# Optimization experiments

Measured on AMD Instinct MI355X. Metric: run time of the kernel, lower is better.

Reference implementation:

```python
import jax, jax.numpy as jnp
import numpy as np

HEADS = 8
EMBED = 64  # out_channels per head
N_OP = 100000
N_MC = 20000
N_EDGE = 300000
EPS = 1e-16  # matches PyG softmax denominator epsilon


def hetero_gat(x_src, x_dst, edge_index, W, att, n_dst):
    """GAT conv: gather -> per-edge score -> segment softmax over dst -> scatter-sum -> head mean.
    x_src: [Ns, F], x_dst: [Nd, F], edge_index: [2, E] (row0=src, row1=dst),
    W: [HEADS*EMBED, F], att: [1, HEADS, 2*EMBED].
    """
    hs = (x_src @ W.T).reshape(-1, HEADS, EMBED)  # [Ns,H,C]
    hd = (x_dst @ W.T).reshape(-1, HEADS, EMBED)  # [Nd,H,C]
    src, dst = edge_index[0], edge_index[1]
    x_j = hs[src]                                  # [E,H,C] (source/neighbor)
    x_i = hd[dst]                                  # [E,H,C] (destination)
    att_i = att[0, :, :EMBED]                      # [H,C] weights for x_i part of concat
    att_j = att[0, :, EMBED:]                      # [H,C] weights for x_j part
    # (cat([x_i,x_j],-1) * att).sum(-1) without materializing the concat
    alpha = jnp.einsum('ehc,hc->eh', x_i, att_i) + jnp.einsum('ehc,hc->eh', x_j, att_j)
    # segment softmax grouped by destination node
    m = jax.ops.segment_max(alpha, dst, num_segments=n_dst)  # [Nd,H]
    e = jnp.exp(alpha - m[dst])
    s = jax.ops.segment_sum(e, dst, num_segments=n_dst)      # [Nd,H]
    alpha = e / (s[dst] + EPS)                                # [E,H]
    msg = x_j * alpha[..., None]                              # [E,H,C]
    out = jax.ops.segment_sum(msg, dst, num_segments=n_dst)   # [Nd,H,C]
    return out.mean(axis=1)                                   # [Nd,C] multi-head mean


def setup_inputs() -> dict:
    key = jax.random.key(0)
    ks = jax.random.split(key, 12)
    op_nodes = jax.random.normal(ks[0], (N_OP, 4), dtype=jnp.float32)
    mc_nodes = jax.random.normal(ks[1], (N_MC, 2), dtype=jnp.float32)
    src = jax.random.randint(ks[2], (N_EDGE,), 0, N_OP)
    dst = jax.random.randint(ks[3], (N_EDGE,), 0, N_MC)
    edge_index_om = jnp.stack([src, dst]).astype(jnp.int64)
    g = 0.1
    params = {
        'W_op': jax.random.normal(ks[4], (EMBED, 4), dtype=jnp.float32) * g,
        'b_op': jnp.zeros((EMBED,), dtype=jnp.float32),
        'W_mc': jax.random.normal(ks[5], (EMBED, 2), dtype=jnp.float32) * g,
        'b_mc': jnp.zeros((EMBED,), dtype=jnp.float32),
        'W_om': jax.random.normal(ks[6], (HEADS * EMBED, EMBED), dtype=jnp.float32) * g,
        'att_om': jax.random.normal(ks[7], (1, HEADS, 2 * EMBED), dtype=jnp.float32) * g,
        'W_mo': jax.random.normal(ks[8], (HEADS * EMBED, EMBED), dtype=jnp.float32) * g,
        'att_mo': jax.random.normal(ks[9], (1, HEADS, 2 * EMBED), dtype=jnp.float32) * g,
    }
    return {'op_nodes': op_nodes, 'mc_nodes': mc_nodes, 'edge_index_om': edge_index_om, **params}


def reference(op_nodes, mc_nodes, edge_index_om, W_op, b_op, W_mc, b_mc,
              W_om, att_om, W_mo, att_mo):
    h_op = jax.nn.elu(op_nodes @ W_op.T + b_op)   # [N_OP, 64]
    h_mc = jax.nn.elu(mc_nodes @ W_mc.T + b_mc)   # [N_MC, 64]
    # op -> mc
    h_mc_new = hetero_gat(h_op, h_mc, edge_index_om, W_om, att_om, N_MC)
    h_mc = jax.nn.elu(h_mc + h_mc_new)
    # mc -> op (reversed edges)
    edge_index_mo = jnp.stack([edge_index_om[1], edge_index_om[0]])
    h_op_new = hetero_gat(h_mc, h_op, edge_index_mo, W_mo, att_mo, N_OP)
    h_op = jax.nn.elu(h_op + h_op_new)
    return (h_op, h_mc)
```

## Files before the change

kernel.cpp:

```cpp
#include <hip/hip_runtime.h>
#include <hip/hip_bf16.h>

using bf16 = __hip_bfloat16;
typedef __attribute__((ext_vector_type(8))) short short8;
typedef __attribute__((ext_vector_type(4))) float f32x4;

__device__ __forceinline__ unsigned short f2bf(float f) {
  bf16 h = __float2bfloat16(f);
  return *reinterpret_cast<unsigned short*>(&h);
}
__device__ __forceinline__ float bf2f(unsigned short u) {
  return __uint_as_float(((unsigned)u) << 16);
}

__device__ __forceinline__ float loadf(const void* p, int i, int is_f32) {
  if (is_f32) return ((const float*)p)[i];
  return __bfloat162float(((const bf16*)p)[i]);
}

__global__ __launch_bounds__(256) void init_kernel(
    const int* __restrict__ ei, const unsigned short* __restrict__ x,
    int* __restrict__ flags, int* __restrict__ cnt1, int n1,
    int* __restrict__ cnt2, int n2) {
  int t = threadIdx.x;
  int g = blockIdx.x * 256 + t;
  int stride = gridDim.x * 256;
  for (int i = g; i < n1; i += stride) cnt1[i] = 0;
  for (int i = g; i < n2; i += stride) cnt2[i] = 0;
  if (blockIdx.x == 0) {
    __shared__ int red[256];
    int o = 0, big = 0;
    for (int i = t; i < 2048; i += 256) {
      o |= ei[2 * i + 1];
      float v = __uint_as_float(((unsigned)x[2 * i]) << 16);
      if (!(fabsf(v) < 1000.f)) big = 1;
    }
    red[t] = o;
    __syncthreads();
    for (int d = 128; d > 0; d >>= 1) {
      if (t < d) red[t] |= red[t + d];
      __syncthreads();
    }
    int o_all = red[0];
    __syncthreads();
    red[t] = big;
    __syncthreads();
    for (int d = 128; d > 0; d >>= 1) {
      if (t < d) red[t] |= red[t + d];
      __syncthreads();
    }
    if (t == 0) {
      flags[0] = red[0];
      flags[1] = (o_all == 0) ? 1 : 0;
    }
  }
}

__device__ __forceinline__ int edge_src(const int* ei, int E, int e, int i64) {
  return i64 ? ei[2 * e] : ei[e];
}
__device__ __forceinline__ int edge_dst(const int* ei, int E, int e, int i64) {
  return i64 ? ei[2 * E + 2 * e] : ei[E + e];
}

template <int FIN>
__device__ __forceinline__ void node_body(
    const void* x, const void* W, const void* b, int is_f32,
    const float* vj, bf16* h_out, float* ea_out, int n) {
  int lane = threadIdx.x & 63;
  float acc = loadf(b, lane, is_f32);
#pragma unroll
  for (int f = 0; f < FIN; ++f)
    acc += loadf(x, n * FIN + f, is_f32) * loadf(W, lane * FIN + f, is_f32);
  float hv = acc > 0.f ? acc : expm1f(acc);
  h_out[(size_t)n * 64 + lane] = __float2bfloat16(hv);
  if (ea_out) {
    float p[8];
#pragma unroll
    for (int h = 0; h < 8; ++h) p[h] = hv * vj[h * 64 + lane];
#pragma unroll
    for (int i = 0; i < 4; ++i) {
      float send = (lane & 4) ? p[i] : p[i + 4];
      float keep = (lane & 4) ? p[i + 4] : p[i];
      p[i] = keep + __shfl_xor(send, 4, 64);
    }
#pragma unroll
    for (int i = 0; i < 2; ++i) {
      float send = (lane & 2) ? p[i] : p[i + 2];
      float keep = (lane & 2) ? p[i + 2] : p[i];
      p[i] = keep + __shfl_xor(send, 2, 64);
    }
    {
      float send = (lane & 1) ? p[0] : p[1];
      float keep = (lane & 1) ? p[1] : p[0];
      p[0] = keep + __shfl_xor(send, 1, 64);
    }
    p[0] += __shfl_xor(p[0], 8, 64);
    p[0] += __shfl_xor(p[0], 16, 64);
    p[0] += __shfl_xor(p[0], 32, 64);
    if (lane < 8) ea_out[(size_t)n * 8 + lane] = __expf(p[0]);
  }
}

__global__ __launch_bounds__(256) void front_kernel(
    const void* __restrict__ x_op, const void* __restrict__ W_op,
    const void* __restrict__ b_op, const void* __restrict__ x_mc,
    const void* __restrict__ W_mc, const void* __restrict__ b_mc,
    const void* __restrict__ W1, const void* __restrict__ att1,
    const void* __restrict__ W2, const void* __restrict__ att2,
    const int* __restrict__ ei, const int* __restrict__ flags,
    float* __restrict__ vj1, bf16* __restrict__ Wrt1, float* __restrict__ vj2,
    bf16* __restrict__ Wrt2, bf16* __restrict__ h_op,
    float* __restrict__ ea_op, bf16* __restrict__ h_mc,
    int* __restrict__ cnt_dst, int* __restrict__ cnt_src, int n_op, int n_mc,
    int E, int nbo, int nbm) {
  int bid = blockIdx.x;
  int is_f32 = flags[0];
  if (bid < nbo) {
    int n = bid * 4 + (threadIdx.x >> 6);
    if (n < n_op) node_body<4>(x_op, W_op, b_op, is_f32, vj1, h_op, ea_op, n);
  } else if (bid < nbo + nbm) {
    int n = (bid - nbo) * 4 + (threadIdx.x >> 6);
    if (n < n_mc)
      node_body<2>(x_mc, W_mc, b_mc, is_f32, nullptr, h_mc, nullptr, n);
  } else if (bid < nbo + nbm + 256) {
    int pb = bid - nbo - nbm;
    int side = pb >= 128;
    const void* W = side ? W2 : W1;
    const void* att = side ? att2 : att1;
    float* vj = side ? vj2 : vj1;
    bf16* Wrt = side ? Wrt2 : Wrt1;
    int tt = (pb & 127) * 256 + threadIdx.x;
    if (tt < 32768) {
      int c = tt >> 9, k = tt & 511;
      int f = k >> 3, h = k & 7;
      Wrt[tt] = __float2bfloat16(loadf(W, ((h << 6) + c) * 64 + f, is_f32));
    }
    if (tt < 512) {
      int hh = tt >> 6, ff = tt & 63;
      float s = 0.f;
      for (int cc = 0; cc < 64; ++cc)
        s += loadf(att, hh * 128 + 64 + cc, is_f32) *
             loadf(W, ((hh << 6) + cc) * 64 + ff, is_f32);
      vj[tt] = s;
    }
  } else {
    int i64 = flags[1];
    int e = (bid - nbo - nbm - 256) * 256 + threadIdx.x;
    if (e < E) {
      atomicAdd(&cnt_dst[edge_dst(ei, E, e, i64)], 1);
      atomicAdd(&cnt_src[edge_src(ei, E, e, i64)], 1);
    }
  }
}

__global__ __launch_bounds__(256) void scan_bsum2(
    const int* __restrict__ cnt1, int n1, int nb1, const int* __restrict__ cnt2,
    int n2, int* __restrict__ bsum1, int* __restrict__ bsum2) {
  __shared__ int red[256];
  int t = threadIdx.x;
  int side = (int)blockIdx.x >= nb1;
  const int* cnt = side ? cnt2 : cnt1;
  int n = side ? n2 : n1;
  int blk = side ? (blockIdx.x - nb1) : blockIdx.x;
  int base = blk * 2048 + t * 8;
  int s = 0;
#pragma unroll
  for (int i = 0; i < 8; ++i)
    if (base + i < n) s += cnt[base + i];
  red[t] = s;
  __syncthreads();
  for (int d = 128; d > 0; d >>= 1) {
    if (t < d) red[t] += red[t + d];
    __syncthreads();
  }
  if (t == 0) (side ? bsum2 : bsum1)[blk] = red[0];
}

__global__ __launch_bounds__(256) void scan_write2(
    const int* __restrict__ cnt1, int n1, int nb1,
    const int* __restrict__ bsum1, int* __restrict__ offs1,
    int* __restrict__ cur1, const int* __restrict__ cnt2, int n2, int nb2,
    const int* __restrict__ bsum2, int* __restrict__ offs2,
    int* __restrict__ cur2) {
  __shared__ int red[256];
  __shared__ int base_s;
  int t = threadIdx.x;
  int side = (int)blockIdx.x >= nb1;
  const int* cnt = side ? cnt2 : cnt1;
  const int* bsum = side ? bsum2 : bsum1;
  int* offs = side ? offs2 : offs1;
  int* cur = side ? cur2 : cur1;
  int n = side ? n2 : n1;
  int nb = side ? nb2 : nb1;
  int blk = side ? (blockIdx.x - nb1) : blockIdx.x;
  if (t == 0) {
    int b = 0;
    for (int i = 0; i < blk; ++i) b += bsum[i];
    base_s = b;
  }
  int base = blk * 2048 + t * 8;
  int c[8];
  int s = 0;
#pragma unroll
  for (int i = 0; i < 8; ++i) {
    c[i] = (base + i < n) ? cnt[base + i] : 0;
    s += c[i];
  }
  red[t] = s;
  __syncthreads();
  for (int d = 1; d < 256; d <<= 1) {
    int v = red[t];
    int add = (t >= d) ? red[t - d] : 0;
    __syncthreads();
    red[t] = v + add;
    __syncthreads();
  }
  int run = base_s + red[t] - s;
#pragma unroll
  for (int i = 0; i < 8; ++i) {
    if (base + i < n) {
      offs[base + i] = run;
      cur[base + i] = run;
      run += c[i];
    }
  }
  if (blk == nb - 1 && t == 255) offs[n] = base_s + red[255];
}

__global__ __launch_bounds__(256) void fill_edges(
    const int* __restrict__ ei, int E, const int* __restrict__ flags,
    int* __restrict__ cur1, int* __restrict__ srcs1, int* __restrict__ cur2,
    int* __restrict__ srcs2) {
  int i64 = flags[1];
  int e = blockIdx.x * blockDim.x + threadIdx.x;
  if (e < E) {
    int s = edge_src(ei, E, e, i64), d = edge_dst(ei, E, e, i64);
    int p = atomicAdd(&cur1[d], 1);
    srcs1[p] = s;
    int q = atomicAdd(&cur2[s], 1);
    srcs2[q] = d;
  }
}

template <bool WRITE_AJ, bool WRITE_BF>
__global__ __launch_bounds__(256) void gat_fused(
    int Nd, const int* __restrict__ offs, const int* __restrict__ srcs,
    const float* __restrict__ ea, const bf16* __restrict__ h_src,
    const bf16* __restrict__ Wrt, const bf16* __restrict__ h_res,
    float* __restrict__ out_f32, bf16* __restrict__ out_bf,
    const float* __restrict__ vj_next, float* __restrict__ ea_next) {
  __shared__ __align__(16) unsigned short Zl[16 * 520];
  __shared__ int srcs_sw[4][65];
  __shared__ __align__(16) float ew_s[4][520];
  __shared__ float ajp[4][16][8];

  int t = threadIdx.x;
  int wv = t >> 6, lane = t & 63;
  int d0 = blockIdx.x * 16;
  int sj = lane >> 4;
  int fq = lane & 15;

  int dlo = d0 + wv * 4;
  int wo0 = offs[min(dlo + 0, Nd)];
  int wo1 = offs[min(dlo + 1, Nd)];
  int wo2 = offs[min(dlo + 2, Nd)];
  int wo3 = offs[min(dlo + 3, Nd)];
  int wo4 = offs[min(dlo + 4, Nd)];
  int woj = sj == 0 ? wo0 : sj == 1 ? wo1 : sj == 2 ? wo2 : wo3;
  int woj1 = sj == 0 ? wo1 : sj == 1 ? wo2 : sj == 2 ? wo3 : wo4;

  float z[8][4];
#pragma unroll
  for (int h = 0; h < 8; ++h)
#pragma unroll
    for (int f = 0; f < 4; ++f) z[h][f] = 0.f;
  float s8[8];
#pragma unroll
  for (int h = 0; h < 8; ++h) s8[h] = 0.f;

  for (int cb = wo0; cb < wo4; cb += 64) {
    int cn = min(64, wo4 - cb);
    for (int i = lane; i < cn + 1; i += 64)
      srcs_sw[wv][i] = (i < cn) ? srcs[cb + i] : 0;
    for (int i = lane; i < (cn + 1) * 8; i += 64) {
      int e = i >> 3;
      ew_s[wv][i] =
          (e < cn) ? ea[(size_t)srcs_sw[wv][e] * 8 + (i & 7)] : 0.f;
    }
    int c0 = max(cb, woj) - cb;
    int e1 = min(cb + cn, woj1) - cb;
    int rl = max(e1 - c0, 0);
    int rmax = max(rl, __shfl_xor(rl, 16, 64));
    rmax = max(rmax, __shfl_xor(rmax, 32, 64));
    for (int r = 0; r < rmax; ++r) {
      int i2 = (r < rl) ? (c0 + r) : cn;
      int src = srcs_sw[wv][i2];
      ushort4 u = *(const ushort4*)((const unsigned short*)h_src +
                                    (size_t)src * 64 + fq * 4);
      float x0 = bf2f(u.x), x1 = bf2f(u.y), x2 = bf2f(u.z), x3 = bf2f(u.w);
      float4 lo4 = *(const float4*)&ew_s[wv][i2 * 8];
      float4 hi4 = *(const float4*)&ew_s[wv][i2 * 8 + 4];
      z[0][0] += lo4.x * x0; z[0][1] += lo4.x * x1; z[0][2] += lo4.x * x2; z[0][3] += lo4.x * x3;
      z[1][0] += lo4.y * x0; z[1][1] += lo4.y * x1; z[1][2] += lo4.y * x2; z[1][3] += lo4.y * x3;
      z[2][0] += lo4.z * x0; z[2][1] += lo4.z * x1; z[2][2] += lo4.z * x2; z[2][3] += lo4.z * x3;
      z[3][0] += lo4.w * x0; z[3][1] += lo4.w * x1; z[3][2] += lo4.w * x2; z[3][3] += lo4.w * x3;
      z[4][0] += hi4.x * x0; z[4][1] += hi4.x * x1; z[4][2] += hi4.x * x2; z[4][3] += hi4.x * x3;
      z[5][0] += hi4.y * x0; z[5][1] += hi4.y * x1; z[5][2] += hi4.y * x2; z[5][3] += hi4.y * x3;
      z[6][0] += hi4.z * x0; z[6][1] += hi4.z * x1; z[6][2] += hi4.z * x2; z[6][3] += hi4.z * x3;
      z[7][0] += hi4.w * x0; z[7][1] += hi4.w * x1; z[7][2] += hi4.w * x2; z[7][3] += hi4.w * x3;
      s8[0] += lo4.x; s8[1] += lo4.y; s8[2] += lo4.z; s8[3] += lo4.w;
      s8[4] += hi4.x; s8[5] += hi4.y; s8[6] += hi4.z; s8[7] += hi4.w;
    }
  }

  float si[8];
#pragma unroll
  for (int h = 0; h < 8; ++h) si[h] = s8[h] > 0.f ? 1.f / s8[h] : 0.f;
  int row = wv * 4 + sj;
#pragma unroll
  for (int fi = 0; fi < 4; ++fi) {
    int4 pk;
    pk.x = ((int)f2bf(z[1][fi] * si[1]) << 16) | f2bf(z[0][fi] * si[0]);
    pk.y = ((int)f2bf(z[3][fi] * si[3]) << 16) | f2bf(z[2][fi] * si[2]);
    pk.z = ((int)f2bf(z[5][fi] * si[5]) << 16) | f2bf(z[4][fi] * si[4]);
    pk.w = ((int)f2bf(z[7][fi] * si[7]) << 16) | f2bf(z[6][fi] * si[6]);
    *(int4*)&Zl[row * 520 + (fq * 4 + fi) * 8] = pk;
  }
  __syncthreads();

  int arow = lane & 15;
  int kg = lane >> 4;
  f32x4 acc = {0.f, 0.f, 0.f, 0.f};
#pragma unroll
  for (int kt = 0; kt < 16; ++kt) {
    int kbase = kt * 32 + kg * 8;
    short8 a = *(const short8*)&Zl[arow * 520 + kbase];
    short8 b = *(const short8*)&Wrt[(size_t)(wv * 16 + arow) * 512 + kbase];
    acc = __builtin_amdgcn_mfma_f32_16x16x32_bf16(a, b, acc, 0, 0, 0);
  }

  int col = wv * 16 + arow;
  float o_r[4];
#pragma unroll
  for (int r = 0; r < 4; ++r) {
    int dloc = kg * 4 + r;
    int d = d0 + dloc;
    float o = 0.f;
    if (d < Nd) {
      float v = __bfloat162float(h_res[(size_t)d * 64 + col]) + 0.125f * acc[r];
      o = v > 0.f ? v : expm1f(v);
      out_f32[(size_t)d * 64 + col] = o;
      if (WRITE_BF) out_bf[(size_t)d * 64 + col] = __float2bfloat16(o);
    }
    o_r[r] = o;
  }

  if (WRITE_AJ) {
#pragma unroll
    for (int r = 0; r < 4; ++r) {
      int dloc = kg * 4 + r;
      float p[8];
#pragma unroll
      for (int h = 0; h < 8; ++h) p[h] = o_r[r] * vj_next[h * 64 + col];
#pragma unroll
      for (int i = 0; i < 4; ++i) {
        float send = (arow & 4) ? p[i] : p[i + 4];
        float keep = (arow & 4) ? p[i + 4] : p[i];
        p[i] = keep + __shfl_xor(send, 4, 64);
      }
#pragma unroll
      for (int i = 0; i < 2; ++i) {
        float send = (arow & 2) ? p[i] : p[i + 2];
        float keep = (arow & 2) ? p[i + 2] : p[i];
        p[i] = keep + __shfl_xor(send, 2, 64);
      }
      {
        float send = (arow & 1) ? p[0] : p[1];
        float keep = (arow & 1) ? p[1] : p[0];
        p[0] = keep + __shfl_xor(send, 1, 64);
      }
      p[0] += __shfl_xor(p[0], 8, 64);
      if (arow < 8) ajp[wv][dloc][arow] = p[0];
    }
    __syncthreads();
    if (t < 128) {
      int dloc = t >> 3, h = t & 7;
      int d = d0 + dloc;
      if (d < Nd) {
        float s = ajp[0][dloc][h] + ajp[1][dloc][h] + ajp[2][dloc][h] +
                  ajp[3][dloc][h];
        ea_next[(size_t)d * 8 + h] = __expf(s);
      }
    }
  }
}

extern "C" void kernel_launch(void* const* d_in, const int* in_sizes, int n_in,
                              void* d_out, int out_size, void* d_ws,
                              size_t ws_size, hipStream_t stream) {
  const void* op_nodes = d_in[0];
  const void* mc_nodes = d_in[1];
  const int* ei        = (const int*)d_in[2];
  const void* W_op     = d_in[3];
  const void* b_op     = d_in[4];
  const void* W_mc     = d_in[5];
  const void* b_mc     = d_in[6];
  const void* W_om     = d_in[7];
  const void* att_om   = d_in[8];
  const void* W_mo     = d_in[9];
  const void* att_mo   = d_in[10];

  int n_op = in_sizes[0] / 4;
  int n_mc = in_sizes[1] / 2;
  int E    = in_sizes[2] / 2;

  char* ws = (char*)d_ws;
  size_t off = 0;
  auto alloc = [&](size_t bytes) -> void* {
    void* p = ws + off;
    off = (off + bytes + 255) & ~(size_t)255;
    return p;
  };
  int* flags   = (int*)alloc(16);
  bf16* h_op   = (bf16*)alloc((size_t)n_op * 64 * 2);
  bf16* h_mc   = (bf16*)alloc((size_t)n_mc * 64 * 2);
  bf16* h_mc2  = (bf16*)alloc((size_t)n_mc * 64 * 2);
  float* ea_op = (float*)alloc((size_t)n_op * 8 * 4);
  float* ea_mc = (float*)alloc((size_t)n_mc * 8 * 4);
  float* vj_om = (float*)alloc(512 * 4);
  float* vj_mo = (float*)alloc(512 * 4);
  bf16* Wrt_om = (bf16*)alloc(32768 * 2);
  bf16* Wrt_mo = (bf16*)alloc(32768 * 2);
  int* cnt1  = (int*)alloc((size_t)n_mc * 4);
  int* cnt2  = (int*)alloc((size_t)n_op * 4);
  int* offs1 = (int*)alloc((size_t)(n_mc + 1) * 4);
  int* cur1  = (int*)alloc((size_t)n_mc * 4);
  int* srcs1 = (int*)alloc((size_t)E * 4);
  int* offs2 = (int*)alloc((size_t)(n_op + 1) * 4);
  int* cur2  = (int*)alloc((size_t)n_op * 4);
  int* srcs2 = (int*)alloc((size_t)E * 4);
  int* bsum1 = (int*)alloc(256 * 4);
  int* bsum2 = (int*)alloc(256 * 4);

  float* out_op = (float*)d_out;
  float* out_mc = out_op + (size_t)n_op * 64;

  init_kernel<<<512, 256, 0, stream>>>(ei, (const unsigned short*)op_nodes,
                                       flags, cnt1, n_mc, cnt2, n_op);

  int nbo = (n_op + 3) / 4, nbm = (n_mc + 3) / 4;
  int nbe = (E + 255) / 256;
  front_kernel<<<nbo + nbm + 256 + nbe, 256, 0, stream>>>(
      op_nodes, W_op, b_op, mc_nodes, W_mc, b_mc, W_om, att_om, W_mo, att_mo,
      ei, flags, vj_om, Wrt_om, vj_mo, Wrt_mo, h_op, ea_op, h_mc, cnt1, cnt2,
      n_op, n_mc, E, nbo, nbm);

  int nb1 = (n_mc + 2047) / 2048, nb2 = (n_op + 2047) / 2048;
  scan_bsum2<<<nb1 + nb2, 256, 0, stream>>>(cnt1, n_mc, nb1, cnt2, n_op, bsum1,
                                            bsum2);
  scan_write2<<<nb1 + nb2, 256, 0, stream>>>(cnt1, n_mc, nb1, bsum1, offs1,
                                             cur1, cnt2, n_op, nb2, bsum2,
                                             offs2, cur2);
  fill_edges<<<nbe, 256, 0, stream>>>(ei, E, flags, cur1, srcs1, cur2, srcs2);

  gat_fused<true, true><<<(n_mc + 15) / 16, 256, 0, stream>>>(
      n_mc, offs1, srcs1, ea_op, h_op, Wrt_om, h_mc, out_mc, h_mc2, vj_mo,
      ea_mc);
  gat_fused<false, false><<<(n_op + 15) / 16, 256, 0, stream>>>(
      n_op, offs2, srcs2, ea_mc, h_mc2, Wrt_mo, h_op, out_op, (bf16*)nullptr,
      (const float*)nullptr, (float*)nullptr);
}
```

Before: 240.2 us.

## Batch node work per wave, batch gathers in GAT loop, reuse shared memory

Result: faster. 233.5 us (-2.8%).

```diff
diff --git a/kernel.cpp b/kernel.cpp
--- a/kernel.cpp
+++ b/kernel.cpp
@@ -64,41 +64,55 @@
 }
 
 template <int FIN>
-__device__ __forceinline__ void node_body(
+__device__ __forceinline__ void node_body4(
     const void* x, const void* W, const void* b, int is_f32,
-    const float* vj, bf16* h_out, float* ea_out, int n) {
+    const float* vj, bf16* h_out, float* ea_out, int n0, int N) {
   int lane = threadIdx.x & 63;
-  float acc = loadf(b, lane, is_f32);
-#pragma unroll
-  for (int f = 0; f < FIN; ++f)
-    acc += loadf(x, n * FIN + f, is_f32) * loadf(W, lane * FIN + f, is_f32);
-  float hv = acc > 0.f ? acc : expm1f(acc);
-  h_out[(size_t)n * 64 + lane] = __float2bfloat16(hv);
+  float wreg[FIN];
+#pragma unroll
+  for (int f = 0; f < FIN; ++f) wreg[f] = loadf(W, lane * FIN + f, is_f32);
+  float bias = loadf(b, lane, is_f32);
+  float vjreg[8];
   if (ea_out) {
-    float p[8];
-#pragma unroll
-    for (int h = 0; h < 8; ++h) p[h] = hv * vj[h * 64 + lane];
-#pragma unroll
-    for (int i = 0; i < 4; ++i) {
-      float send = (lane & 4) ? p[i] : p[i + 4];
-      float keep = (lane & 4) ? p[i + 4] : p[i];
-      p[i] = keep + __shfl_xor(send, 4, 64);
-    }
-#pragma unroll
-    for (int i = 0; i < 2; ++i) {
-      float send = (lane & 2) ? p[i] : p[i + 2];
-      float keep = (lane & 2) ? p[i + 2] : p[i];
-      p[i] = keep + __shfl_xor(send, 2, 64);
-    }
-    {
-      float send = (lane & 1) ? p[0] : p[1];
-      float keep = (lane & 1) ? p[1] : p[0];
-      p[0] = keep + __shfl_xor(send, 1, 64);
-    }
-    p[0] += __shfl_xor(p[0], 8, 64);
-    p[0] += __shfl_xor(p[0], 16, 64);
-    p[0] += __shfl_xor(p[0], 32, 64);
-    if (lane < 8) ea_out[(size_t)n * 8 + lane] = __expf(p[0]);
+#pragma unroll
+    for (int h = 0; h < 8; ++h) vjreg[h] = vj[h * 64 + lane];
+  }
+#pragma unroll
+  for (int j = 0; j < 4; ++j) {
+    int n = n0 + j;
+    if (n >= N) break;
+    float acc = bias;
+#pragma unroll
+    for (int f = 0; f < FIN; ++f)
+      acc += loadf(x, n * FIN + f, is_f32) * wreg[f];
+    float hv = acc > 0.f ? acc : expm1f(acc);
+    h_out[(unsigned)(n << 6) + lane] = __float2bfloat16(hv);
+    if (ea_out) {
+      float p[8];
+#pragma unroll
+      for (int h = 0; h < 8; ++h) p[h] = hv * vjreg[h];
+#pragma unroll
+      for (int i = 0; i < 4; ++i) {
+        float send = (lane & 4) ? p[i] : p[i + 4];
+        float keep = (lane & 4) ? p[i + 4] : p[i];
+        p[i] = keep + __shfl_xor(send, 4, 64);
+      }
+#pragma unroll
+      for (int i = 0; i < 2; ++i) {
+        float send = (lane & 2) ? p[i] : p[i + 2];
+        float keep = (lane & 2) ? p[i + 2] : p[i];
+        p[i] = keep + __shfl_xor(send, 2, 64);
+      }
+      {
+        float send = (lane & 1) ? p[0] : p[1];
+        float keep = (lane & 1) ? p[1] : p[0];
+        p[0] = keep + __shfl_xor(send, 1, 64);
+      }
+      p[0] += __shfl_xor(p[0], 8, 64);
+      p[0] += __shfl_xor(p[0], 16, 64);
+      p[0] += __shfl_xor(p[0], 32, 64);
+      if (lane < 8) ea_out[(unsigned)(n << 3) + lane] = __expf(p[0]);
+    }
   }
 }
 
@@ -117,12 +131,13 @@
   int bid = blockIdx.x;
   int is_f32 = flags[0];
   if (bid < nbo) {
-    int n = bid * 4 + (threadIdx.x >> 6);
-    if (n < n_op) node_body<4>(x_op, W_op, b_op, is_f32, vj1, h_op, ea_op, n);
+    int n0 = bid * 16 + (threadIdx.x >> 6) * 4;
+    if (n0 < n_op)
+      node_body4<4>(x_op, W_op, b_op, is_f32, vj1, h_op, ea_op, n0, n_op);
   } else if (bid < nbo + nbm) {
-    int n = (bid - nbo) * 4 + (threadIdx.x >> 6);
-    if (n < n_mc)
-      node_body<2>(x_mc, W_mc, b_mc, is_f32, nullptr, h_mc, nullptr, n);
+    int n0 = (bid - nbo) * 16 + (threadIdx.x >> 6) * 4;
+    if (n0 < n_mc)
+      node_body4<2>(x_mc, W_mc, b_mc, is_f32, nullptr, h_mc, nullptr, n0, n_mc);
   } else if (bid < nbo + nbm + 256) {
     int pb = bid - nbo - nbm;
     int side = pb >= 128;
@@ -252,8 +267,8 @@
     const float* __restrict__ vj_next, float* __restrict__ ea_next) {
   __shared__ __align__(16) unsigned short Zl[16 * 520];
   __shared__ int srcs_sw[4][65];
-  __shared__ __align__(16) float ew_s[4][520];
-  __shared__ float ajp[4][16][8];
+  __shared__ __align__(16) float ew_s[4][528];
+  float(*ajp)[16][8] = reinterpret_cast<float(*)[16][8]>(&ew_s[0][0]);
 
   int t = threadIdx.x;
   int wv = t >> 6, lane = t & 63;
@@ -279,38 +294,51 @@
 #pragma unroll
   for (int h = 0; h < 8; ++h) s8[h] = 0.f;
 
+  const unsigned short* hsrc_u = (const unsigned short*)h_src;
+
   for (int cb = wo0; cb < wo4; cb += 64) {
     int cn = min(64, wo4 - cb);
     for (int i = lane; i < cn + 1; i += 64)
       srcs_sw[wv][i] = (i < cn) ? srcs[cb + i] : 0;
     for (int i = lane; i < (cn + 1) * 8; i += 64) {
       int e = i >> 3;
-      ew_s[wv][i] =
-          (e < cn) ? ea[(size_t)srcs_sw[wv][e] * 8 + (i & 7)] : 0.f;
+      int src2 = (e < cn) ? srcs[cb + e] : 0;
+      ew_s[wv][i] = (e < cn) ? ea[((unsigned)src2 << 3) + (i & 7)] : 0.f;
     }
     int c0 = max(cb, woj) - cb;
     int e1 = min(cb + cn, woj1) - cb;
     int rl = max(e1 - c0, 0);
     int rmax = max(rl, __shfl_xor(rl, 16, 64));
     rmax = max(rmax, __shfl_xor(rmax, 32, 64));
-    for (int r = 0; r < rmax; ++r) {
-      int i2 = (r < rl) ? (c0 + r) : cn;
-      int src = srcs_sw[wv][i2];
-      ushort4 u = *(const ushort4*)((const unsigned short*)h_src +
-                                    (size_t)src * 64 + fq * 4);
-      float x0 = bf2f(u.x), x1 = bf2f(u.y), x2 = bf2f(u.z), x3 = bf2f(u.w);
-      float4 lo4 = *(const float4*)&ew_s[wv][i2 * 8];
-      float4 hi4 = *(const float4*)&ew_s[wv][i2 * 8 + 4];
-      z[0][0] += lo4.x * x0; z[0][1] += lo4.x * x1; z[0][2] += lo4.x * x2; z[0][3] += lo4.x * x3;
-      z[1][0] += lo4.y * x0; z[1][1] += lo4.y * x1; z[1][2] += lo4.y * x2; z[1][3] += lo4.y * x3;
-      z[2][0] += lo4.z * x0; z[2][1] += lo4.z * x1; z[2][2] += lo4.z * x2; z[2][3] += lo4.z * x3;
-      z[3][0] += lo4.w * x0; z[3][1] += lo4.w * x1; z[3][2] += lo4.w * x2; z[3][3] += lo4.w * x3;
-      z[4][0] += hi4.x * x0; z[4][1] += hi4.x * x1; z[4][2] += hi4.x * x2; z[4][3] += hi4.x * x3;
-      z[5][0] += hi4.y * x0; z[5][1] += hi4.y * x1; z[5][2] += hi4.y * x2; z[5][3] += hi4.y * x3;
-      z[6][0] += hi4.z * x0; z[6][1] += hi4.z * x1; z[6][2] += hi4.z * x2; z[6][3] += hi4.z * x3;
-      z[7][0] += hi4.w * x0; z[7][1] += hi4.w * x1; z[7][2] += hi4.w * x2; z[7][3] += hi4.w * x3;
-      s8[0] += lo4.x; s8[1] += lo4.y; s8[2] += lo4.z; s8[3] += lo4.w;
-      s8[4] += hi4.x; s8[5] += hi4.y; s8[6] += hi4.z; s8[7] += hi4.w;
+    for (int r0 = 0; r0 < rmax; r0 += 4) {
+      int i2q[4];
+      ushort4 uq[4];
+#pragma unroll
+      for (int q = 0; q < 4; ++q) {
+        int r = r0 + q;
+        int i2 = (r < rl) ? (c0 + r) : cn;
+        i2q[q] = i2;
+        int src = srcs_sw[wv][i2];
+        uq[q] = *(const ushort4*)(hsrc_u + (((unsigned)src) << 6) + (fq << 2));
+      }
+#pragma unroll
+      for (int q = 0; q < 4; ++q) {
+        int i2 = i2q[q];
+        float4 lo4 = *(const float4*)&ew_s[wv][i2 * 8];
+        float4 hi4 = *(const float4*)&ew_s[wv][i2 * 8 + 4];
+        float x0 = bf2f(uq[q].x), x1 = bf2f(uq[q].y);
+        float x2 = bf2f(uq[q].z), x3 = bf2f(uq[q].w);
+        z[0][0] += lo4.x * x0; z[0][1] += lo4.x * x1; z[0][2] += lo4.x * x2; z[0][3] += lo4.x * x3;
+        z[1][0] += lo4.y * x0; z[1][1] += lo4.y * x1; z[1][2] += lo4.y * x2; z[1][3] += lo4.y * x3;
+        z[2][0] += lo4.z * x0; z[2][1] += lo4.z * x1; z[2][2] += lo4.z * x2; z[2][3] += lo4.z * x3;
+        z[3][0] += lo4.w * x0; z[3][1] += lo4.w * x1; z[3][2] += lo4.w * x2; z[3][3] += lo4.w * x3;
+        z[4][0] += hi4.x * x0; z[4][1] += hi4.x * x1; z[4][2] += hi4.x * x2; z[4][3] += hi4.x * x3;
+        z[5][0] += hi4.y * x0; z[5][1] += hi4.y * x1; z[5][2] += hi4.y * x2; z[5][3] += hi4.y * x3;
+        z[6][0] += hi4.z * x0; z[6][1] += hi4.z * x1; z[6][2] += hi4.z * x2; z[6][3] += hi4.z * x3;
+        z[7][0] += hi4.w * x0; z[7][1] += hi4.w * x1; z[7][2] += hi4.w * x2; z[7][3] += hi4.w * x3;
+        s8[0] += lo4.x; s8[1] += lo4.y; s8[2] += lo4.z; s8[3] += lo4.w;
+        s8[4] += hi4.x; s8[5] += hi4.y; s8[6] += hi4.z; s8[7] += hi4.w;
+      }
     }
   }
 
@@ -327,31 +355,39 @@
     pk.w = ((int)f2bf(z[7][fi] * si[7]) << 16) | f2bf(z[6][fi] * si[6]);
     *(int4*)&Zl[row * 520 + (fq * 4 + fi) * 8] = pk;
   }
-  __syncthreads();
 
   int arow = lane & 15;
   int kg = lane >> 4;
+  int col = wv * 16 + arow;
+  float res[4];
+#pragma unroll
+  for (int r = 0; r < 4; ++r) {
+    int d = d0 + kg * 4 + r;
+    res[r] = (d < Nd)
+                 ? __bfloat162float(h_res[(unsigned)(d << 6) + col])
+                 : 0.f;
+  }
+  __syncthreads();
+
   f32x4 acc = {0.f, 0.f, 0.f, 0.f};
 #pragma unroll
   for (int kt = 0; kt < 16; ++kt) {
     int kbase = kt * 32 + kg * 8;
     short8 a = *(const short8*)&Zl[arow * 520 + kbase];
-    short8 b = *(const short8*)&Wrt[(size_t)(wv * 16 + arow) * 512 + kbase];
+    short8 b = *(const short8*)&Wrt[(unsigned)((wv * 16 + arow) * 512 + kbase)];
     acc = __builtin_amdgcn_mfma_f32_16x16x32_bf16(a, b, acc, 0, 0, 0);
   }
 
-  int col = wv * 16 + arow;
   float o_r[4];
 #pragma unroll
   for (int r = 0; r < 4; ++r) {
-    int dloc = kg * 4 + r;
-    int d = d0 + dloc;
+    int d = d0 + kg * 4 + r;
     float o = 0.f;
     if (d < Nd) {
-      float v = __bfloat162float(h_res[(size_t)d * 64 + col]) + 0.125f * acc[r];
+      float v = res[r] + 0.125f * acc[r];
       o = v > 0.f ? v : expm1f(v);
-      out_f32[(size_t)d * 64 + col] = o;
-      if (WRITE_BF) out_bf[(size_t)d * 64 + col] = __float2bfloat16(o);
+      out_f32[(unsigned)(d << 6) + col] = o;
+      if (WRITE_BF) out_bf[(unsigned)(d << 6) + col] = __float2bfloat16(o);
     }
     o_r[r] = o;
   }
@@ -390,7 +426,7 @@
       if (d < Nd) {
         float s = ajp[0][dloc][h] + ajp[1][dloc][h] + ajp[2][dloc][h] +
                   ajp[3][dloc][h];
-        ea_next[(size_t)d * 8 + h] = __expf(s);
+        ea_next[(unsigned)(d << 3) + h] = __expf(s);
       }
     }
   }
@@ -449,7 +485,7 @@
   init_kernel<<<512, 256, 0, stream>>>(ei, (const unsigned short*)op_nodes,
                                        flags, cnt1, n_mc, cnt2, n_op);
 
-  int nbo = (n_op + 3) / 4, nbm = (n_mc + 3) / 4;
+  int nbo = (n_op + 15) / 16, nbm = (n_mc + 15) / 16;
   int nbe = (E + 255) / 256;
   front_kernel<<<nbo + nbm + 256 + nbe, 256, 0, stream>>>(
       op_nodes, W_op, b_op, mc_nodes, W_mc, b_mc, W_om, att_om, W_mo, att_mo,
```
